# Performance work log

Hardware: AMD Instinct MI355X
Metric: run time of the kernel (lower is better)

## Reference

```python
import jax, jax.numpy as jnp
import numpy as np

MARGIN = 0.3
EPS_DIST = 1e-12   # clamp before sqrt, as in torch source
EPS_PAIR = 1e-6    # torch F.pairwise_distance eps added to the difference


def setup_inputs() -> dict:
    key = jax.random.key(0)
    k1, k2 = jax.random.split(key)
    n, d = 8192, 256
    inputs = jax.random.normal(k1, (n, d), dtype=jnp.float32)
    positive = jax.random.normal(k2, (n, d), dtype=jnp.float32)
    return {"inputs": inputs, "positive": positive}


def reference(inputs, positive):
    # Pairwise Euclidean distances: ||xi||^2 + ||xj||^2 - 2 xi.xj
    sq = jnp.sum(inputs * inputs, axis=1)                      # [n]
    dist = sq[:, None] + sq[None, :] - 2.0 * (inputs @ inputs.T)  # [n, n]
    dist = jnp.sqrt(jnp.clip(dist, EPS_DIST))
    # 3rd-smallest per row (index 2 of argsort); row i's smallest is itself.
    _, idx3 = jax.lax.top_k(-dist, 3)                          # [n, 3]
    negative = inputs[idx3[:, 2]]                              # [n, d] gather
    # TripletMarginLoss(margin, p=2): mean(relu(d(a,p) - d(a,n) + margin))
    d_ap = jnp.linalg.norm(inputs - positive + EPS_PAIR, axis=1)
    d_an = jnp.linalg.norm(inputs - negative + EPS_PAIR, axis=1)
    return jnp.mean(jnp.maximum(d_ap - d_an + MARGIN, 0.0))
```

## Files before the change

### kernel.cpp

```cpp
#include <hip/hip_runtime.h>
#include <math.h>

#define N 8192
#define D 256
#define NCH 32
#define RB 256
#define RT 4
#define CHUNK (N / NCH)
#define NCT (CHUNK / 16)

constexpr float MARGIN = 0.3f;
constexpr float EPS_PAIR = 1e-6f;
constexpr float BIAS = 512.0f;

typedef float f32x4 __attribute__((ext_vector_type(4)));
typedef int   i32x8 __attribute__((ext_vector_type(8)));

__device__ __forceinline__ void load_lds16(const void* g, void* l) {
  __builtin_amdgcn_global_load_lds((const __attribute__((address_space(1))) void*)g,
                                   (__attribute__((address_space(3))) void*)l, 16, 0, 0);
}

__device__ __forceinline__ void top2merge(unsigned& v1, unsigned& v2,
                                          unsigned w1, unsigned w2) {
  unsigned mx = v1 > w1 ? v1 : w1;
  v1 = v1 < w1 ? v1 : w1;
  unsigned mn = v2 < w2 ? v2 : w2;
  v2 = mx < mn ? mx : mn;
}

__global__ void prep_kernel(const float* __restrict__ in, char* __restrict__ A8,
                            float* __restrict__ sqh) {
  int row  = blockIdx.x * 4 + (threadIdx.x >> 6);
  int lane = threadIdx.x & 63;
  float4 v = ((const float4*)(in + (size_t)row * D))[lane];
  int w = 0;
  w = __builtin_amdgcn_cvt_pk_fp8_f32(v.x, v.y, w, false);
  w = __builtin_amdgcn_cvt_pk_fp8_f32(v.z, v.w, w, true);
  *(int*)(A8 + (size_t)row * D + lane * 4) = w;
  float s = v.x * v.x + v.y * v.y + v.z * v.z + v.w * v.w;
#pragma unroll
  for (int m = 32; m; m >>= 1) s += __shfl_xor(s, m);
  if (lane == 0) sqh[row] = -0.5f * (s + BIAS);
}

__global__ __launch_bounds__(256, 3) void neighbor_kernel(
    const char* __restrict__ A8, const float* __restrict__ sqh,
    uint2* __restrict__ pp) {
  __shared__ __attribute__((aligned(32))) char ldsB[2][4096];
  __shared__ float ldsSq[CHUNK];

  const int t = threadIdx.x;
  const int lane = t & 63;
  const int wave = t >> 6;
  const int rowBase = blockIdx.x * RB + wave * 64;
  const int colBase = blockIdx.y * CHUNK;

  const int lrow = lane & 15;
  const int lkg  = lane >> 4;

  i32x8 afrag[RT][2];
#pragma unroll
  for (int rt = 0; rt < RT; ++rt) {
    const char* arow = A8 + (size_t)(rowBase + rt * 16 + lrow) * D;
#pragma unroll
    for (int ks = 0; ks < 2; ++ks)
      afrag[rt][ks] = *(const i32x8*)(arow + ks * 128 + lkg * 32);
  }

  for (int i = t; i < CHUNK; i += 256) ldsSq[i] = sqh[colBase + i];

  int dsoff[2];
#pragma unroll
  for (int ks = 0; ks < 2; ++ks)
    dsoff[ks] = lrow * 256 + ((ks * 128 + lkg * 32) ^ ((lrow & 7) << 5));

  const int pw = wave * 1024 + lane * 16;
  const char* src;
  {
    int r = pw >> 8, o = pw & 255;
    src = A8 + (size_t)(colBase + r) * 256 + (o ^ ((r & 7) << 5));
  }

  unsigned v1[RT][4], v2[RT][4];
#pragma unroll
  for (int rt = 0; rt < RT; ++rt)
#pragma unroll
    for (int q = 0; q < 4; ++q) { v1[rt][q] = 0xFFFFFFFFu; v2[rt][q] = 0xFFFFFFFFu; }

  load_lds16(src, &ldsB[0][pw]); src += 4096;
  __syncthreads();

#define BODY(CT, BUF)                                                          \
  {                                                                            \
    if ((CT) + 1 < NCT) { load_lds16(src, &ldsB[(BUF) ^ 1][pw]); src += 4096; }\
    const float sqv = ldsSq[(CT) * 16 + lrow];                                 \
    f32x4 acc[RT];                                                             \
    _Pragma("unroll")                                                          \
    for (int rt = 0; rt < RT; ++rt) acc[rt] = (f32x4){sqv, sqv, sqv, sqv};     \
    const char* bt = ldsB[BUF];                                                \
    _Pragma("unroll")                                                          \
    for (int ks = 0; ks < 2; ++ks) {                                           \
      i32x8 bfrag = *(const i32x8*)(bt + dsoff[ks]);                           \
      _Pragma("unroll")                                                        \
      for (int rt = 0; rt < RT; ++rt)                                          \
        acc[rt] = __builtin_amdgcn_mfma_scale_f32_16x16x128_f8f6f4(            \
            afrag[rt][ks], bfrag, acc[rt], 0, 0,                               \
            0, 0x7F7F7F7F, 0, 0x7F7F7F7F);                                     \
    }                                                                          \
    const int j = colBase + (CT) * 16 + lrow;                                  \
    _Pragma("unroll")                                                          \
    for (int rt = 0; rt < RT; ++rt) {                                          \
      const bool diag = (colBase + (CT) * 16) == (rowBase + rt * 16);          \
      _Pragma("unroll")                                                        \
      for (int q = 0; q < 4; ++q) {                                            \
        unsigned p = (__float_as_uint(acc[rt][q]) & 0xFFFFE000u) | (unsigned)j;\
        if (diag) p = (lrow == lkg * 4 + q) ? 0xFFFFFFFFu : p;                 \
        unsigned nv1 = v1[rt][q] < p ? v1[rt][q] : p;                          \
        unsigned mx  = p > v1[rt][q] ? p : v1[rt][q];                          \
        v2[rt][q] = v2[rt][q] < mx ? v2[rt][q] : mx;                           \
        v1[rt][q] = nv1;                                                       \
      }                                                                        \
    }                                                                          \
    __syncthreads();                                                           \
  }

#pragma unroll 1
  for (int ct = 0; ct < NCT; ct += 2) {
    BODY(ct, 0)
    BODY(ct + 1, 1)
  }
#undef BODY

#pragma unroll
  for (int rt = 0; rt < RT; ++rt) {
#pragma unroll
    for (int q = 0; q < 4; ++q) {
      unsigned a1 = v1[rt][q], a2 = v2[rt][q];
#pragma unroll
      for (int m = 1; m < 16; m <<= 1) {
        unsigned w1 = (unsigned)__shfl_xor((int)a1, m);
        unsigned w2 = (unsigned)__shfl_xor((int)a2, m);
        top2merge(a1, a2, w1, w2);
      }
      if (lrow == 0) {
        int ig = rowBase + rt * 16 + lkg * 4 + q;
        pp[(size_t)blockIdx.y * N + ig] = make_uint2(a1, a2);
      }
    }
  }
}

__global__ void finish_kernel(const float* __restrict__ A, const float* __restrict__ P,
                              const uint2* __restrict__ pp, float* __restrict__ rowLoss) {
  int row  = blockIdx.x * 4 + (threadIdx.x >> 6);
  int lane = threadIdx.x & 63;

  uint2 pr = pp[(size_t)(lane & 31) * N + row];
  unsigned a1 = pr.x, a2 = pr.y;
#pragma unroll
  for (int m = 1; m < 32; m <<= 1) {
    unsigned w1 = (unsigned)__shfl_xor((int)a1, m);
    unsigned w2 = (unsigned)__shfl_xor((int)a2, m);
    top2merge(a1, a2, w1, w2);
  }
  int nr = (int)(a2 & 0x1FFFu);

  float4 av = ((const float4*)(A + (size_t)row * D))[lane];
  float4 pv = ((const float4*)(P + (size_t)row * D))[lane];
  float4 gv = ((const float4*)(A + (size_t)nr  * D))[lane];
  float dap = 0.f, dan = 0.f, x;
  x = av.x - pv.x + EPS_PAIR; dap += x * x;
  x = av.y - pv.y + EPS_PAIR; dap += x * x;
  x = av.z - pv.z + EPS_PAIR; dap += x * x;
  x = av.w - pv.w + EPS_PAIR; dap += x * x;
  x = av.x - gv.x + EPS_PAIR; dan += x * x;
  x = av.y - gv.y + EPS_PAIR; dan += x * x;
  x = av.z - gv.z + EPS_PAIR; dan += x * x;
  x = av.w - gv.w + EPS_PAIR; dan += x * x;
#pragma unroll
  for (int m = 32; m; m >>= 1) {
    dap += __shfl_xor(dap, m);
    dan += __shfl_xor(dan, m);
  }
  if (lane == 0)
    rowLoss[row] = fmaxf(sqrtf(dap) - sqrtf(dan) + MARGIN, 0.f);
}

__global__ void reduce_kernel(const float* __restrict__ rowLoss, float* __restrict__ out) {
  __shared__ float smem[256];
  int t = threadIdx.x;
  float s = 0.f;
  for (int i = t; i < N; i += 256) s += rowLoss[i];
  smem[t] = s;
  __syncthreads();
  for (int stride = 128; stride; stride >>= 1) {
    if (t < stride) smem[t] += smem[t + stride];
    __syncthreads();
  }
  if (t == 0) out[0] = smem[0] * (1.0f / (float)N);
}

extern "C" void kernel_launch(void* const* d_in, const int* in_sizes, int n_in,
                              void* d_out, int out_size, void* d_ws, size_t ws_size,
                              hipStream_t stream) {
  const float* inputs   = (const float*)d_in[0];
  const float* positive = (const float*)d_in[1];
  float* out = (float*)d_out;

  char*  A8      = (char*)d_ws;
  float* sqh     = (float*)(A8 + (size_t)N * D);
  uint2* pp      = (uint2*)(sqh + N);
  float* rowLoss = (float*)(pp + (size_t)NCH * N);

  prep_kernel<<<N / 4, 256, 0, stream>>>(inputs, A8, sqh);
  neighbor_kernel<<<dim3(N / RB, NCH), 256, 0, stream>>>(A8, sqh, pp);
  finish_kernel<<<N / 4, 256, 0, stream>>>(inputs, positive, pp, rowLoss);
  reduce_kernel<<<1, 256, 0, stream>>>(rowLoss, out);
}
```

Baseline: 56.51 us.

## Load B fragments directly from global into registers, dropping LDS staging

Replaces the LDS double-buffered global_load_lds staging of column tiles and its per-tile __syncthreads with direct per-wave global loads of B fragments into registers. Even and odd tiles are prefetched one step ahead, with wrap-around so the last prefetch stays in bounds. This removes the barriers and LDS traffic, but each wave now fetches B redundantly from L2/global instead of sharing one block-wide copy, which raises global load traffic and exposes more latency per tile.

```diff
diff --git a/kernel.cpp b/kernel.cpp
--- a/kernel.cpp
+++ b/kernel.cpp
@@ -15,11 +15,6 @@
 
 typedef float f32x4 __attribute__((ext_vector_type(4)));
 typedef int   i32x8 __attribute__((ext_vector_type(8)));
-
-__device__ __forceinline__ void load_lds16(const void* g, void* l) {
-  __builtin_amdgcn_global_load_lds((const __attribute__((address_space(1))) void*)g,
-                                   (__attribute__((address_space(3))) void*)l, 16, 0, 0);
-}
 
 __device__ __forceinline__ void top2merge(unsigned& v1, unsigned& v2,
                                           unsigned w1, unsigned w2) {
@@ -47,7 +42,6 @@
 __global__ __launch_bounds__(256, 3) void neighbor_kernel(
     const char* __restrict__ A8, const float* __restrict__ sqh,
     uint2* __restrict__ pp) {
-  __shared__ __attribute__((aligned(32))) char ldsB[2][4096];
   __shared__ float ldsSq[CHUNK];
 
   const int t = threadIdx.x;
@@ -69,18 +63,7 @@
   }
 
   for (int i = t; i < CHUNK; i += 256) ldsSq[i] = sqh[colBase + i];
-
-  int dsoff[2];
-#pragma unroll
-  for (int ks = 0; ks < 2; ++ks)
-    dsoff[ks] = lrow * 256 + ((ks * 128 + lkg * 32) ^ ((lrow & 7) << 5));
-
-  const int pw = wave * 1024 + lane * 16;
-  const char* src;
-  {
-    int r = pw >> 8, o = pw & 255;
-    src = A8 + (size_t)(colBase + r) * 256 + (o ^ ((r & 7) << 5));
-  }
+  __syncthreads();
 
   unsigned v1[RT][4], v2[RT][4];
 #pragma unroll
@@ -88,33 +71,23 @@
 #pragma unroll
     for (int q = 0; q < 4; ++q) { v1[rt][q] = 0xFFFFFFFFu; v2[rt][q] = 0xFFFFFFFFu; }
 
-  load_lds16(src, &ldsB[0][pw]); src += 4096;
-  __syncthreads();
-
-#define BODY(CT, BUF)                                                          \
+  const char* pE = A8 + (size_t)(colBase + lrow) * 256 + lkg * 32;
+  const char* pO = pE + 4096;
+
+  i32x8 bE0 = *(const i32x8*)(pE);
+  i32x8 bE1 = *(const i32x8*)(pE + 128);
+  i32x8 bO0 = *(const i32x8*)(pO);
+  i32x8 bO1 = *(const i32x8*)(pO + 128);
+
+#define SELECT(CT, ACC)                                                        \
   {                                                                            \
-    if ((CT) + 1 < NCT) { load_lds16(src, &ldsB[(BUF) ^ 1][pw]); src += 4096; }\
-    const float sqv = ldsSq[(CT) * 16 + lrow];                                 \
-    f32x4 acc[RT];                                                             \
-    _Pragma("unroll")                                                          \
-    for (int rt = 0; rt < RT; ++rt) acc[rt] = (f32x4){sqv, sqv, sqv, sqv};     \
-    const char* bt = ldsB[BUF];                                                \
-    _Pragma("unroll")                                                          \
-    for (int ks = 0; ks < 2; ++ks) {                                           \
-      i32x8 bfrag = *(const i32x8*)(bt + dsoff[ks]);                           \
-      _Pragma("unroll")                                                        \
-      for (int rt = 0; rt < RT; ++rt)                                          \
-        acc[rt] = __builtin_amdgcn_mfma_scale_f32_16x16x128_f8f6f4(            \
-            afrag[rt][ks], bfrag, acc[rt], 0, 0,                               \
-            0, 0x7F7F7F7F, 0, 0x7F7F7F7F);                                     \
-    }                                                                          \
     const int j = colBase + (CT) * 16 + lrow;                                  \
     _Pragma("unroll")                                                          \
     for (int rt = 0; rt < RT; ++rt) {                                          \
       const bool diag = (colBase + (CT) * 16) == (rowBase + rt * 16);          \
       _Pragma("unroll")                                                        \
       for (int q = 0; q < 4; ++q) {                                            \
-        unsigned p = (__float_as_uint(acc[rt][q]) & 0xFFFFE000u) | (unsigned)j;\
+        unsigned p = (__float_as_uint(ACC[rt][q]) & 0xFFFFE000u) | (unsigned)j;\
         if (diag) p = (lrow == lkg * 4 + q) ? 0xFFFFFFFFu : p;                 \
         unsigned nv1 = v1[rt][q] < p ? v1[rt][q] : p;                          \
         unsigned mx  = p > v1[rt][q] ? p : v1[rt][q];                          \
@@ -122,15 +95,49 @@
         v1[rt][q] = nv1;                                                       \
       }                                                                        \
     }                                                                          \
-    __syncthreads();                                                           \
-  }
-
-#pragma unroll 1
+  }
+
   for (int ct = 0; ct < NCT; ct += 2) {
-    BODY(ct, 0)
-    BODY(ct + 1, 1)
-  }
-#undef BODY
+    {
+      const float sqv = ldsSq[ct * 16 + lrow];
+      f32x4 acc[RT];
+#pragma unroll
+      for (int rt = 0; rt < RT; ++rt) acc[rt] = (f32x4){sqv, sqv, sqv, sqv};
+#pragma unroll
+      for (int rt = 0; rt < RT; ++rt)
+        acc[rt] = __builtin_amdgcn_mfma_scale_f32_16x16x128_f8f6f4(
+            afrag[rt][0], bE0, acc[rt], 0, 0, 0, 0x7F7F7F7F, 0, 0x7F7F7F7F);
+#pragma unroll
+      for (int rt = 0; rt < RT; ++rt)
+        acc[rt] = __builtin_amdgcn_mfma_scale_f32_16x16x128_f8f6f4(
+            afrag[rt][1], bE1, acc[rt], 0, 0, 0, 0x7F7F7F7F, 0, 0x7F7F7F7F);
+      pE += 8192;
+      if (ct + 2 >= NCT) pE -= CHUNK * 256;
+      bE0 = *(const i32x8*)(pE);
+      bE1 = *(const i32x8*)(pE + 128);
+      SELECT(ct, acc)
+    }
+    {
+      const float sqv = ldsSq[(ct + 1) * 16 + lrow];
+      f32x4 acc[RT];
+#pragma unroll
+      for (int rt = 0; rt < RT; ++rt) acc[rt] = (f32x4){sqv, sqv, sqv, sqv};
+#pragma unroll
+      for (int rt = 0; rt < RT; ++rt)
+        acc[rt] = __builtin_amdgcn_mfma_scale_f32_16x16x128_f8f6f4(
+            afrag[rt][0], bO0, acc[rt], 0, 0, 0, 0x7F7F7F7F, 0, 0x7F7F7F7F);
+#pragma unroll
+      for (int rt = 0; rt < RT; ++rt)
+        acc[rt] = __builtin_amdgcn_mfma_scale_f32_16x16x128_f8f6f4(
+            afrag[rt][1], bO1, acc[rt], 0, 0, 0, 0x7F7F7F7F, 0, 0x7F7F7F7F);
+      pO += 8192;
+      if (ct + 3 >= NCT) pO -= CHUNK * 256;
+      bO0 = *(const i32x8*)(pO);
+      bO1 = *(const i32x8*)(pO + 128);
+      SELECT(ct + 1, acc)
+    }
+  }
+#undef SELECT
 
 #pragma unroll
   for (int rt = 0; rt < RT; ++rt) {
```

Result: slower. 70.14 us (+24.1%).
